# Performance work log

Measured on AMD Instinct MI355X. Metric: run time of the kernel, lower is better.

Reference implementation:

```python
import jax, jax.numpy as jnp
import numpy as np

B_SZ, C_DIM, N_DIM, S_DIM, L = 4, 512, 512, 64, 8192


def setup_inputs() -> dict:
    key = jax.random.key(0)
    ks = jax.random.split(key, 6)
    inp = jax.random.normal(ks[0], (B_SZ, C_DIM, L), dtype=jnp.float32)
    # dtA_real must be negative (exponential decay) so exp(dtA_real * l) stays bounded for l up to L
    dtA_real = -jax.random.uniform(ks[1], (N_DIM, S_DIM), dtype=jnp.float32, minval=1e-4, maxval=1e-2)
    dtA_imag = jax.random.uniform(ks[2], (N_DIM, S_DIM), dtype=jnp.float32, minval=0.0, maxval=0.1)
    Bm = jax.random.normal(ks[3], (N_DIM, C_DIM), dtype=jnp.float32) / np.float32(np.sqrt(C_DIM))
    Cm = jax.random.normal(ks[4], (C_DIM, N_DIM), dtype=jnp.float32) / np.float32(np.sqrt(N_DIM))
    E = jax.random.normal(ks[5], (N_DIM, S_DIM), dtype=jnp.float32) / np.float32(np.sqrt(S_DIM))
    return {"input": inp, "dtA_real": dtA_real, "dtA_imag": dtA_imag, "B": Bm, "C": Cm, "E": E}


def _synth_kernel(dtA_real, dtA_imag, E, length):
    # _K with complex_proj=False, weight=E, dim=-2:
    # K[n, s, l] = exp(dtA_real[n,s] * l) * cos(dtA_imag[n,s] * l); reduce over s with weight E.
    lrange = jnp.arange(length, dtype=jnp.float32)
    K = jnp.exp(dtA_real[..., None] * lrange) * jnp.cos(dtA_imag[..., None] * lrange)  # [n, s, L]
    return jnp.sum(K * E[..., None], axis=-2)  # [n, L]


def _fft_conv_dw(u, k, n):
    # real FFT causal (zero-padded to 2n) depthwise convolution: y = irfft(rfft(u) * rfft(k))[:n]
    uf = jnp.fft.rfft(u, 2 * n)          # [b, n, n+1] complex
    kf = jnp.fft.rfft(k, 2 * n)          # [n, n+1] complex, broadcast over batch
    return jnp.fft.irfft(uf * kf, 2 * n)[..., :n]


def reference(input, dtA_real, dtA_imag, B, C, E):
    n = input.shape[-1]
    # kernel synthesis (cached + detached in the torch module)
    K = jax.lax.stop_gradient(_synth_kernel(dtA_real, dtA_imag, E, n))  # [n_dim, L]
    x = jnp.einsum('bcl,nc->bnl', input, B)   # input projection
    x = _fft_conv_dw(x, K, n)                  # depthwise long conv
    return jnp.einsum('bnl,dn->bdl', x, C)     # output projection
```

## Files before the change

kernel.cpp:

```cpp
#include <hip/hip_runtime.h>
#include <hip/hip_bf16.h>

typedef unsigned short u16;
typedef __attribute__((ext_vector_type(8))) short short8;
typedef __attribute__((ext_vector_type(8))) unsigned short ushort8v;
typedef __attribute__((ext_vector_type(4))) float floatx4;

#define BSZ   4
#define CDIM  512
#define NDIM  512
#define SDIM  64
#define LEN   8192

__device__ __forceinline__ u16 f2bf(float x) {
    unsigned int u = __float_as_uint(x);
    unsigned int r = (u + 0x7FFFu + ((u >> 16) & 1u)) >> 16;
    return (u16)r;
}

#define GLL16(g, l)                                                          \
    __builtin_amdgcn_global_load_lds(                                        \
        (const __attribute__((address_space(1))) unsigned int*)(g),          \
        (__attribute__((address_space(3))) unsigned int*)(l), 16, 0, 0)

__global__ __launch_bounds__(256) void prep_nw(const float* __restrict__ dAr,
                                               const float* __restrict__ dAi,
                                               const float* __restrict__ E,
                                               u16* __restrict__ Af,
                                               u16* __restrict__ WW,
                                               const float* __restrict__ Bmf,
                                               const float* __restrict__ Cmf,
                                               u16* __restrict__ bh,
                                               u16* __restrict__ ch) {
    __shared__ float sA[64], sW[64], sE[64];
    __shared__ float Ms[128][65];
    __shared__ float sK[128];
    const int n = blockIdx.x;
    const int t = threadIdx.x;
    if (t < 64) {
        sA[t] = dAr[n * 64 + t];
        sW[t] = dAi[n * 64 + t];
        sE[t] = E[n * 64 + t];
    }
    {
        int i = n * 512 + t * 2;
        float2 vb = *(const float2*)&Bmf[i];
        float2 vc = *(const float2*)&Cmf[i];
        ushort2 hb, hc;
        hb.x = f2bf(vb.x); hb.y = f2bf(vb.y);
        hc.x = f2bf(vc.x); hc.y = f2bf(vc.y);
        *(ushort2*)&bh[i] = hb;
        *(ushort2*)&ch[i] = hc;
    }
    __syncthreads();
    u16* Afn = Af + (size_t)n * 32768;
#pragma unroll 4
    for (int it = 0; it < 32; ++it) {
        int idx = it * 256 + t;
        int tt = idx >> 6, s = idx & 63;
        float a = sA[s], w = sW[s], e = sE[s];
        float tp1 = (float)(tt + 1);
        float sn, cs;
        __sincosf(w * tp1, &sn, &cs);
        float ea = __expf(a * tp1) * e;
        float mr = ea * cs;
        Ms[tt][s] = mr;
        Afn[tt * 256 + 128 + s] = f2bf(mr);
        Afn[tt * 256 + 192 + s] = f2bf(-ea * sn);
    }
    __syncthreads();
    if (t < 128) {
        float acc = 0.f;
        if (t == 0) {
#pragma unroll
            for (int s = 0; s < 64; ++s) acc += sE[s];
        } else {
#pragma unroll
            for (int s = 0; s < 64; ++s) acc += Ms[t - 1][s];
        }
        sK[t] = acc;
    }
    __syncthreads();
#pragma unroll 8
    for (int it = 0; it < 64; ++it) {
        int idx = it * 256 + t;
        int tt = idx >> 7, k = idx & 127;
        float v = (k <= tt) ? sK[tt - k] : 0.f;
        Afn[tt * 256 + k] = f2bf(v);
    }
    u16* WWn = WW + (size_t)n * 16384;
#pragma unroll 4
    for (int it = 0; it < 32; ++it) {
        int idx = it * 256 + t;
        int s = idx >> 7, tau = idx & 127;
        float a = sA[s], w = sW[s];
        float d = (float)(127 - tau);
        float sn, cs;
        __sincosf(w * d, &sn, &cs);
        float ea = __expf(a * d);
        WWn[s * 128 + tau] = f2bf(ea * cs);
        WWn[(s + 64) * 128 + tau] = f2bf(ea * sn);
    }
}

__global__ __launch_bounds__(256) void transpose_in(const float* __restrict__ src,
                                                    u16* __restrict__ dst) {
    __shared__ float tile[64][65];
    const int b  = blockIdx.z;
    const int r0 = blockIdx.y * 64;
    const int c0 = blockIdx.x * 64;
    const int t  = threadIdx.x;
    const float* s = src + (size_t)b * 512 * 8192;
#pragma unroll
    for (int p = 0; p < 4; ++p) {
        int r = (t >> 4) + p * 16;
        float4 v = *(const float4*)&s[(size_t)(r0 + r) * 8192 + c0 + (t & 15) * 4];
        tile[r][(t & 15) * 4 + 0] = v.x;
        tile[r][(t & 15) * 4 + 1] = v.y;
        tile[r][(t & 15) * 4 + 2] = v.z;
        tile[r][(t & 15) * 4 + 3] = v.w;
    }
    __syncthreads();
#pragma unroll
    for (int p = 0; p < 4; ++p) {
        int i  = (t >> 4) + p * 16;
        int cb = (t & 15) * 4;
        ushort4 h;
        u16* hp = (u16*)&h;
#pragma unroll
        for (int q = 0; q < 4; ++q) hp[q] = f2bf(tile[cb + q][i]);
        *(ushort4*)&dst[((size_t)b * 8192 + c0 + i) * 512 + r0 + cb] = h;
    }
}

__global__ __launch_bounds__(256) void transpose_u16(const u16* __restrict__ src,
                                                     u16* __restrict__ dst) {
    __shared__ u16 tile[64][72];
    const int b  = blockIdx.z;
    const int n0 = blockIdx.y * 64;
    const int l0 = blockIdx.x * 64;
    const int t  = threadIdx.x;
    const u16* s = src + (size_t)b * 512 * 8192;
    u16* d = dst + (size_t)b * 8192 * 512;
#pragma unroll
    for (int p = 0; p < 2; ++p) {
        int r = (t >> 3) + p * 32;
        *(ushort8v*)&tile[r][(t & 7) * 8] =
            *(const ushort8v*)&s[(size_t)(n0 + r) * 8192 + l0 + (t & 7) * 8];
    }
    __syncthreads();
#pragma unroll
    for (int p = 0; p < 2; ++p) {
        int li = (t >> 3) + p * 32;
        int cb = (t & 7) * 8;
        ushort8v v;
#pragma unroll
        for (int q = 0; q < 8; ++q) v[q] = tile[cb + q][li];
        *(ushort8v*)&d[(size_t)(l0 + li) * 512 + n0 + cb] = v;
    }
}

__global__ __launch_bounds__(256) void gemm_bf16_o16(const u16* __restrict__ A,
                                                     const u16* __restrict__ Xt,
                                                     u16* __restrict__ Y) {
    __shared__ u16 As[128 * 64];
    __shared__ u16 Xs[128 * 64];
    const int b    = blockIdx.z;
    const int m0   = blockIdx.y * 128;
    const int l0   = blockIdx.x * 128;
    const int t    = threadIdx.x;
    const int w    = t >> 6;
    const int lane = t & 63;
    const int mq   = (w >> 1) * 64;
    const int lq   = (w & 1) * 64;
    const u16* Xb = Xt + (size_t)b * 8192 * 512;
    const int scol = (((lane & 7) ^ (lane >> 3)) << 3);
    const size_t a_off = (size_t)(m0 + 32 * w + (lane >> 3)) * 512 + scol;
    const size_t x_off = (size_t)(l0 + 32 * w + (lane >> 3)) * 512 + scol;
    u16* AsW = As + w * 2048;
    u16* XsW = Xs + w * 2048;

    floatx4 acc[4][4];
#pragma unroll
    for (int i = 0; i < 4; ++i)
#pragma unroll
        for (int j = 0; j < 4; ++j) acc[i][j] = (floatx4)0.f;
    const int fr = lane & 15;
    const int fk = (lane >> 4) * 8;
    const int swz = (fr & 7) << 3;

    for (int k0 = 0; k0 < 512; k0 += 64) {
        __syncthreads();
#pragma unroll
        for (int g = 0; g < 4; ++g) {
            GLL16(A + a_off + g * 4096 + k0, AsW + g * 512);
            GLL16(Xb + x_off + g * 4096 + k0, XsW + g * 512);
        }
        __syncthreads();
#pragma unroll
        for (int kk = 0; kk < 64; kk += 32) {
            short8 af[4], bf[4];
            const int pc = (kk + fk) ^ swz;
#pragma unroll
            for (int i = 0; i < 4; ++i) {
                af[i] = *(const short8*)&As[(mq + i * 16 + fr) * 64 + pc];
                bf[i] = *(const short8*)&Xs[(lq + i * 16 + fr) * 64 + pc];
            }
#pragma unroll
            for (int i = 0; i < 4; ++i)
#pragma unroll
                for (int j = 0; j < 4; ++j)
                    acc[i][j] = __builtin_amdgcn_mfma_f32_16x16x32_bf16(
                        af[i], bf[j], acc[i][j], 0, 0, 0);
        }
    }
    u16* Yb = Y + (size_t)b * 512 * 8192;
#pragma unroll
    for (int i = 0; i < 4; ++i)
#pragma unroll
        for (int j = 0; j < 4; ++j)
#pragma unroll
            for (int r = 0; r < 4; ++r) {
                int mg = m0 + mq + i * 16 + (lane >> 4) * 4 + r;
                int lg = l0 + lq + j * 16 + (lane & 15);
                Yb[(size_t)mg * 8192 + lg] = f2bf(acc[i][j][r]);
            }
}

__global__ __launch_bounds__(256) void gemm_bf16_o32(const u16* __restrict__ A,
                                                     const u16* __restrict__ Xt,
                                                     float* __restrict__ Y) {
    __shared__ u16 As[128 * 64];
    __shared__ u16 Xs[128 * 64];
    const int b    = blockIdx.z;
    const int m0   = blockIdx.y * 128;
    const int l0   = blockIdx.x * 128;
    const int t    = threadIdx.x;
    const int w    = t >> 6;
    const int lane = t & 63;
    const int mq   = (w >> 1) * 64;
    const int lq   = (w & 1) * 64;
    const u16* Xb = Xt + (size_t)b * 8192 * 512;
    const int scol = (((lane & 7) ^ (lane >> 3)) << 3);
    const size_t a_off = (size_t)(m0 + 32 * w + (lane >> 3)) * 512 + scol;
    const size_t x_off = (size_t)(l0 + 32 * w + (lane >> 3)) * 512 + scol;
    u16* AsW = As + w * 2048;
    u16* XsW = Xs + w * 2048;

    floatx4 acc[4][4];
#pragma unroll
    for (int i = 0; i < 4; ++i)
#pragma unroll
        for (int j = 0; j < 4; ++j) acc[i][j] = (floatx4)0.f;
    const int fr = lane & 15;
    const int fk = (lane >> 4) * 8;
    const int swz = (fr & 7) << 3;

    for (int k0 = 0; k0 < 512; k0 += 64) {
        __syncthreads();
#pragma unroll
        for (int g = 0; g < 4; ++g) {
            GLL16(A + a_off + g * 4096 + k0, AsW + g * 512);
            GLL16(Xb + x_off + g * 4096 + k0, XsW + g * 512);
        }
        __syncthreads();
#pragma unroll
        for (int kk = 0; kk < 64; kk += 32) {
            short8 af[4], bf[4];
            const int pc = (kk + fk) ^ swz;
#pragma unroll
            for (int i = 0; i < 4; ++i) {
                af[i] = *(const short8*)&As[(mq + i * 16 + fr) * 64 + pc];
                bf[i] = *(const short8*)&Xs[(lq + i * 16 + fr) * 64 + pc];
            }
#pragma unroll
            for (int i = 0; i < 4; ++i)
#pragma unroll
                for (int j = 0; j < 4; ++j)
                    acc[i][j] = __builtin_amdgcn_mfma_f32_16x16x32_bf16(
                        af[i], bf[j], acc[i][j], 0, 0, 0);
        }
    }
    float* Yb = Y + (size_t)b * 512 * 8192;
#pragma unroll
    for (int i = 0; i < 4; ++i)
#pragma unroll
        for (int j = 0; j < 4; ++j)
#pragma unroll
            for (int r = 0; r < 4; ++r) {
                int mg = m0 + mq + i * 16 + (lane >> 4) * 4 + r;
                int lg = l0 + lq + j * 16 + (lane & 15);
                Yb[(size_t)mg * 8192 + lg] = acc[i][j][r];
            }
}

__global__ __launch_bounds__(256) void se_gemm(const u16* __restrict__ xbf,
                                               const u16* __restrict__ WW,
                                               u16* __restrict__ SEf) {
    __shared__ u16 As[128 * 32];
    __shared__ u16 Bs[128 * 32];
    const int n  = blockIdx.y;
    const int c0 = blockIdx.x * 128;
    const int t  = threadIdx.x;
    const int w  = t >> 6, lane = t & 63;
    const int mq = (w >> 1) * 64;
    const int lq = (w & 1) * 64;
    const int ar0 = 32 * w + (lane >> 2);
    const int kq8 = (lane & 3) * 8;
    const int c_a0 = c0 + ar0, c_a1 = c_a0 + 16;
    const size_t xrow0 = ((size_t)(c_a0 >> 6) * 512 + n) * 8192 + (size_t)(c_a0 & 63) * 128 + kq8;
    const size_t xrow1 = ((size_t)(c_a1 >> 6) * 512 + n) * 8192 + (size_t)(c_a1 & 63) * 128 + kq8;
    const size_t brow0 = (size_t)n * 16384 + (size_t)ar0 * 128 + kq8;
    const size_t brow1 = brow0 + 16 * 128;
    const int wofs = w * 1024;

    floatx4 acc[4][4];
#pragma unroll
    for (int i = 0; i < 4; ++i)
#pragma unroll
        for (int j = 0; j < 4; ++j) acc[i][j] = (floatx4)0.f;
    const int fr = lane & 15, fk = (lane >> 4) * 8;

    for (int k0 = 0; k0 < 128; k0 += 32) {
        __syncthreads();
        GLL16(xbf + xrow0 + k0, As + wofs);
        GLL16(xbf + xrow1 + k0, As + wofs + 512);
        GLL16(WW + brow0 + k0, Bs + wofs);
        GLL16(WW + brow1 + k0, Bs + wofs + 512);
        __syncthreads();
        short8 af[4], bf[4];
#pragma unroll
        for (int i = 0; i < 4; ++i) {
            af[i] = *(const short8*)&As[(mq + i * 16 + fr) * 32 + fk];
            bf[i] = *(const short8*)&Bs[(lq + i * 16 + fr) * 32 + fk];
        }
#pragma unroll
        for (int i = 0; i < 4; ++i)
#pragma unroll
            for (int j = 0; j < 4; ++j)
                acc[i][j] = __builtin_amdgcn_mfma_f32_16x16x32_bf16(
                    af[i], bf[j], acc[i][j], 0, 0, 0);
    }
#pragma unroll
    for (int i = 0; i < 4; ++i)
#pragma unroll
        for (int j = 0; j < 4; ++j)
#pragma unroll
            for (int r = 0; r < 4; ++r) {
                int c = c0 + mq + i * 16 + (lane >> 4) * 4 + r;
                int q = lq + j * 16 + (lane & 15);
                SEf[(((size_t)(c >> 6) * 512 + n) * 64 + (c & 63)) * 128 + q] =
                    f2bf(acc[i][j][r]);
            }
}

__global__ __launch_bounds__(256) void bscan(const float* __restrict__ dAr,
                                             const float* __restrict__ dAi,
                                             const u16* __restrict__ SEf,
                                             u16* __restrict__ Ht) {
    const int id = blockIdx.x * 256 + threadIdx.x;
    const int s = id & 63, n = (id >> 6) & 511, b = id >> 15;
    const float a = dAr[n * 64 + s], wv = dAi[n * 64 + s];
    const float eaT = expf(a * 128.f);
    float sT, cT;
    sincosf(wv * 128.f, &sT, &cT);
    const float zTr = eaT * cT, zTi = eaT * sT;
    const size_t base = ((size_t)b * 512 + n) * 64 * 128;
    float Hr = 0.f, Hi = 0.f;
    for (int j = 0; j < 64; ++j) {
        Ht[base + j * 128 + s]      = f2bf(Hr);
        Ht[base + j * 128 + 64 + s] = f2bf(Hi);
        float ser = __uint_as_float((unsigned int)SEf[base + j * 128 + s] << 16);
        float sei = __uint_as_float((unsigned int)SEf[base + j * 128 + 64 + s] << 16);
        float nHr = fmaf(zTr, Hr, fmaf(-zTi, Hi, ser));
        float nHi = fmaf(zTi, Hr, fmaf(zTr, Hi, sei));
        Hr = nHr; Hi = nHi;
    }
}

__global__ __launch_bounds__(256) void y_gemm(const u16* __restrict__ xbf,
                                              const u16* __restrict__ Ht,
                                              const u16* __restrict__ Af,
                                              u16* __restrict__ wyb) {
    __shared__ u16 As[128 * 32];
    __shared__ u16 Bs[128 * 32];
    const int n  = blockIdx.y;
    const int c0 = blockIdx.x * 128;
    const int t  = threadIdx.x;
    const int w  = t >> 6, lane = t & 63;
    const int mq = (w >> 1) * 64;
    const int lq = (w & 1) * 64;
    const int ar0 = 32 * w + (lane >> 2);
    const int kq8 = (lane & 3) * 8;
    const int c_a0 = c0 + ar0, c_a1 = c_a0 + 16;
    const size_t xrow0 = ((size_t)(c_a0 >> 6) * 512 + n) * 8192 + (size_t)(c_a0 & 63) * 128 + kq8;
    const size_t xrow1 = ((size_t)(c_a1 >> 6) * 512 + n) * 8192 + (size_t)(c_a1 & 63) * 128 + kq8;
    const size_t hrow0 = (((size_t)(c_a0 >> 6) * 512 + n) * 64 + (c_a0 & 63)) * 128 + kq8;
    const size_t hrow1 = (((size_t)(c_a1 >> 6) * 512 + n) * 64 + (c_a1 & 63)) * 128 + kq8;
    const size_t brow0 = (size_t)n * 32768 + (size_t)ar0 * 256 + kq8;
    const size_t brow1 = brow0 + 16 * 256;
    const int wofs = w * 1024;

    floatx4 acc[4][4];
#pragma unroll
    for (int i = 0; i < 4; ++i)
#pragma unroll
        for (int j = 0; j < 4; ++j) acc[i][j] = (floatx4)0.f;
    const int fr = lane & 15, fk = (lane >> 4) * 8;

    for (int k0 = 0; k0 < 256; k0 += 32) {
        __syncthreads();
        if (k0 < 128) {
            GLL16(xbf + xrow0 + k0, As + wofs);
            GLL16(xbf + xrow1 + k0, As + wofs + 512);
        } else {
            GLL16(Ht + hrow0 + (k0 - 128), As + wofs);
            GLL16(Ht + hrow1 + (k0 - 128), As + wofs + 512);
        }
        GLL16(Af + brow0 + k0, Bs + wofs);
        GLL16(Af + brow1 + k0, Bs + wofs + 512);
        __syncthreads();
        short8 af[4], bf[4];
#pragma unroll
        for (int i = 0; i < 4; ++i) {
            af[i] = *(const short8*)&As[(mq + i * 16 + fr) * 32 + fk];
            bf[i] = *(const short8*)&Bs[(lq + i * 16 + fr) * 32 + fk];
        }
#pragma unroll
        for (int i = 0; i < 4; ++i)
#pragma unroll
            for (int j = 0; j < 4; ++j)
                acc[i][j] = __builtin_amdgcn_mfma_f32_16x16x32_bf16(
                    af[i], bf[j], acc[i][j], 0, 0, 0);
    }
#pragma unroll
    for (int i = 0; i < 4; ++i)
#pragma unroll
        for (int j = 0; j < 4; ++j)
#pragma unroll
            for (int r = 0; r < 4; ++r) {
                int c  = c0 + mq + i * 16 + (lane >> 4) * 4 + r;
                int tc = lq + j * 16 + (lane & 15);
                wyb[((size_t)(c >> 6) * 512 + n) * 8192 + (size_t)(c & 63) * 128 + tc] =
                    f2bf(acc[i][j][r]);
            }
}

extern "C" void kernel_launch(void* const* d_in, const int* in_sizes, int n_in,
                              void* d_out, int out_size, void* d_ws, size_t ws_size,
                              hipStream_t stream) {
    const float* input = (const float*)d_in[0];
    const float* dAr   = (const float*)d_in[1];
    const float* dAi   = (const float*)d_in[2];
    const float* Bm    = (const float*)d_in[3];
    const float* Cm    = (const float*)d_in[4];
    const float* E     = (const float*)d_in[5];
    float* out = (float*)d_out;

    char* ws = (char*)d_ws;
    const size_t MB = 1048576;
    u16* xt   = (u16*)(ws + 0);
    u16* xbf  = (u16*)(ws + 32 * MB);
    u16* Af   = (u16*)(ws + 64 * MB);
    u16* WW   = (u16*)(ws + 96 * MB);
    u16* SEf  = (u16*)(ws + 112 * MB);
    u16* Ht   = (u16*)(ws + 144 * MB);
    u16* Bmb  = (u16*)(ws + 176 * MB);
    u16* Cmb  = (u16*)(ws + 177 * MB);
    u16* wyb  = xt;
    u16* yt   = xbf;

    prep_nw<<<512, 256, 0, stream>>>(dAr, dAi, E, Af, WW, Bm, Cm, Bmb, Cmb);
    transpose_in<<<dim3(128, 8, BSZ), 256, 0, stream>>>(input, xt);
    gemm_bf16_o16<<<dim3(64, 4, BSZ), 256, 0, stream>>>(Bmb, xt, xbf);
    se_gemm<<<dim3(2, 512), 256, 0, stream>>>(xbf, WW, SEf);
    bscan<<<512, 256, 0, stream>>>(dAr, dAi, SEf, Ht);
    y_gemm<<<dim3(2, 512), 256, 0, stream>>>(xbf, Ht, Af, wyb);
    transpose_u16<<<dim3(128, 8, BSZ), 256, 0, stream>>>(wyb, yt);
    gemm_bf16_o32<<<dim3(64, 4, BSZ), 256, 0, stream>>>(Cmb, yt, out);
}
```

Measured before the change: 268.1 us.

## Merge prep with input transpose and double M tile in se/y GEMMs

Folds the parameter-prep kernel and the input transpose into one launch, dispatching on block index, so one kernel launch and its tail are removed. Doubles the per-block M tile in se_gemm and y_gemm from 128 to 256 rows (8x4 accumulators per wave), so each B tile loaded into LDS is reused twice as much and the grid shrinks from 1024 to 512 blocks. The trade is higher register pressure, lower occupancy and fewer blocks in flight.

```diff
diff --git a/kernel.cpp b/kernel.cpp
--- a/kernel.cpp
+++ b/kernel.cpp
@@ -23,113 +23,118 @@
         (const __attribute__((address_space(1))) unsigned int*)(g),          \
         (__attribute__((address_space(3))) unsigned int*)(l), 16, 0, 0)
 
-__global__ __launch_bounds__(256) void prep_nw(const float* __restrict__ dAr,
-                                               const float* __restrict__ dAi,
-                                               const float* __restrict__ E,
-                                               u16* __restrict__ Af,
-                                               u16* __restrict__ WW,
-                                               const float* __restrict__ Bmf,
-                                               const float* __restrict__ Cmf,
-                                               u16* __restrict__ bh,
-                                               u16* __restrict__ ch) {
-    __shared__ float sA[64], sW[64], sE[64];
-    __shared__ float Ms[128][65];
-    __shared__ float sK[128];
-    const int n = blockIdx.x;
+__global__ __launch_bounds__(256) void prep_all(const float* __restrict__ dAr,
+                                                const float* __restrict__ dAi,
+                                                const float* __restrict__ E,
+                                                u16* __restrict__ Af,
+                                                u16* __restrict__ WW,
+                                                const float* __restrict__ Bmf,
+                                                const float* __restrict__ Cmf,
+                                                u16* __restrict__ bh,
+                                                u16* __restrict__ ch,
+                                                const float* __restrict__ input,
+                                                u16* __restrict__ xt) {
+    __shared__ __align__(16) char smem[34816];
+    const int bid = blockIdx.x;
     const int t = threadIdx.x;
-    if (t < 64) {
-        sA[t] = dAr[n * 64 + t];
-        sW[t] = dAi[n * 64 + t];
-        sE[t] = E[n * 64 + t];
-    }
-    {
-        int i = n * 512 + t * 2;
-        float2 vb = *(const float2*)&Bmf[i];
-        float2 vc = *(const float2*)&Cmf[i];
-        ushort2 hb, hc;
-        hb.x = f2bf(vb.x); hb.y = f2bf(vb.y);
-        hc.x = f2bf(vc.x); hc.y = f2bf(vc.y);
-        *(ushort2*)&bh[i] = hb;
-        *(ushort2*)&ch[i] = hc;
-    }
-    __syncthreads();
-    u16* Afn = Af + (size_t)n * 32768;
+    if (bid < 512) {
+        float* sA = (float*)smem;
+        float* sW = sA + 64;
+        float* sE = sW + 64;
+        float* sK = sE + 64;
+        float (*Ms)[65] = (float (*)[65])(sK + 128);
+        const int n = bid;
+        if (t < 64) {
+            sA[t] = dAr[n * 64 + t];
+            sW[t] = dAi[n * 64 + t];
+            sE[t] = E[n * 64 + t];
+        }
+        {
+            int i = n * 512 + t * 2;
+            float2 vb = *(const float2*)&Bmf[i];
+            float2 vc = *(const float2*)&Cmf[i];
+            ushort2 hb, hc;
+            hb.x = f2bf(vb.x); hb.y = f2bf(vb.y);
+            hc.x = f2bf(vc.x); hc.y = f2bf(vc.y);
+            *(ushort2*)&bh[i] = hb;
+            *(ushort2*)&ch[i] = hc;
+        }
+        __syncthreads();
+        u16* Afn = Af + (size_t)n * 32768;
 #pragma unroll 4
-    for (int it = 0; it < 32; ++it) {
-        int idx = it * 256 + t;
-        int tt = idx >> 6, s = idx & 63;
-        float a = sA[s], w = sW[s], e = sE[s];
-        float tp1 = (float)(tt + 1);
-        float sn, cs;
-        __sincosf(w * tp1, &sn, &cs);
-        float ea = __expf(a * tp1) * e;
-        float mr = ea * cs;
-        Ms[tt][s] = mr;
-        Afn[tt * 256 + 128 + s] = f2bf(mr);
-        Afn[tt * 256 + 192 + s] = f2bf(-ea * sn);
-    }
-    __syncthreads();
-    if (t < 128) {
-        float acc = 0.f;
-        if (t == 0) {
-#pragma unroll
-            for (int s = 0; s < 64; ++s) acc += sE[s];
-        } else {
-#pragma unroll
-            for (int s = 0; s < 64; ++s) acc += Ms[t - 1][s];
-        }
-        sK[t] = acc;
-    }
-    __syncthreads();
+        for (int it = 0; it < 32; ++it) {
+            int idx = it * 256 + t;
+            int tt = idx >> 6, s = idx & 63;
+            float a = sA[s], w = sW[s], e = sE[s];
+            float tp1 = (float)(tt + 1);
+            float sn, cs;
+            __sincosf(w * tp1, &sn, &cs);
+            float ea = __expf(a * tp1) * e;
+            float mr = ea * cs;
+            Ms[tt][s] = mr;
+            Afn[tt * 256 + 128 + s] = f2bf(mr);
+            Afn[tt * 256 + 192 + s] = f2bf(-ea * sn);
+        }
+        __syncthreads();
+        if (t < 128) {
+            float acc = 0.f;
+            if (t == 0) {
+#pragma unroll
+                for (int s = 0; s < 64; ++s) acc += sE[s];
+            } else {
+#pragma unroll
+                for (int s = 0; s < 64; ++s) acc += Ms[t - 1][s];
+            }
+            sK[t] = acc;
+        }
+        __syncthreads();
 #pragma unroll 8
-    for (int it = 0; it < 64; ++it) {
-        int idx = it * 256 + t;
-        int tt = idx >> 7, k = idx & 127;
-        float v = (k <= tt) ? sK[tt - k] : 0.f;
-        Afn[tt * 256 + k] = f2bf(v);
-    }
-    u16* WWn = WW + (size_t)n * 16384;
+        for (int it = 0; it < 64; ++it) {
+            int idx = it * 256 + t;
+            int tt = idx >> 7, k = idx & 127;
+            float v = (k <= tt) ? sK[tt - k] : 0.f;
+            Afn[tt * 256 + k] = f2bf(v);
+        }
+        u16* WWn = WW + (size_t)n * 16384;
 #pragma unroll 4
-    for (int it = 0; it < 32; ++it) {
-        int idx = it * 256 + t;
-        int s = idx >> 7, tau = idx & 127;
-        float a = sA[s], w = sW[s];
-        float d = (float)(127 - tau);
-        float sn, cs;
-        __sincosf(w * d, &sn, &cs);
-        float ea = __expf(a * d);
-        WWn[s * 128 + tau] = f2bf(ea * cs);
-        WWn[(s + 64) * 128 + tau] = f2bf(ea * sn);
-    }
-}
-
-__global__ __launch_bounds__(256) void transpose_in(const float* __restrict__ src,
-                                                    u16* __restrict__ dst) {
-    __shared__ float tile[64][65];
-    const int b  = blockIdx.z;
-    const int r0 = blockIdx.y * 64;
-    const int c0 = blockIdx.x * 64;
-    const int t  = threadIdx.x;
-    const float* s = src + (size_t)b * 512 * 8192;
-#pragma unroll
-    for (int p = 0; p < 4; ++p) {
-        int r = (t >> 4) + p * 16;
-        float4 v = *(const float4*)&s[(size_t)(r0 + r) * 8192 + c0 + (t & 15) * 4];
-        tile[r][(t & 15) * 4 + 0] = v.x;
-        tile[r][(t & 15) * 4 + 1] = v.y;
-        tile[r][(t & 15) * 4 + 2] = v.z;
-        tile[r][(t & 15) * 4 + 3] = v.w;
-    }
-    __syncthreads();
-#pragma unroll
-    for (int p = 0; p < 4; ++p) {
-        int i  = (t >> 4) + p * 16;
-        int cb = (t & 15) * 4;
-        ushort4 h;
-        u16* hp = (u16*)&h;
-#pragma unroll
-        for (int q = 0; q < 4; ++q) hp[q] = f2bf(tile[cb + q][i]);
-        *(ushort4*)&dst[((size_t)b * 8192 + c0 + i) * 512 + r0 + cb] = h;
+        for (int it = 0; it < 32; ++it) {
+            int idx = it * 256 + t;
+            int s = idx >> 7, tau = idx & 127;
+            float a = sA[s], w = sW[s];
+            float d = (float)(127 - tau);
+            float sn, cs;
+            __sincosf(w * d, &sn, &cs);
+            float ea = __expf(a * d);
+            WWn[s * 128 + tau] = f2bf(ea * cs);
+            WWn[(s + 64) * 128 + tau] = f2bf(ea * sn);
+        }
+    } else {
+        float (*tile)[65] = (float (*)[65])smem;
+        const int tid = bid - 512;
+        const int b  = tid >> 10;
+        const int r0 = ((tid >> 7) & 7) * 64;
+        const int c0 = (tid & 127) * 64;
+        const float* s = input + (size_t)b * 512 * 8192;
+#pragma unroll
+        for (int p = 0; p < 4; ++p) {
+            int r = (t >> 4) + p * 16;
+            float4 v = *(const float4*)&s[(size_t)(r0 + r) * 8192 + c0 + (t & 15) * 4];
+            tile[r][(t & 15) * 4 + 0] = v.x;
+            tile[r][(t & 15) * 4 + 1] = v.y;
+            tile[r][(t & 15) * 4 + 2] = v.z;
+            tile[r][(t & 15) * 4 + 3] = v.w;
+        }
+        __syncthreads();
+#pragma unroll
+        for (int p = 0; p < 4; ++p) {
+            int i  = (t >> 4) + p * 16;
+            int cb = (t & 15) * 4;
+            ushort4 h;
+            u16* hp = (u16*)&h;
+#pragma unroll
+            for (int q = 0; q < 4; ++q) hp[q] = f2bf(tile[cb + q][i]);
+            *(ushort4*)&xt[((size_t)b * 8192 + c0 + i) * 512 + r0 + cb] = h;
+        }
     }
 }
 
@@ -297,58 +302,62 @@
 __global__ __launch_bounds__(256) void se_gemm(const u16* __restrict__ xbf,
                                                const u16* __restrict__ WW,
                                                u16* __restrict__ SEf) {
-    __shared__ u16 As[128 * 32];
+    __shared__ u16 As[256 * 32];
     __shared__ u16 Bs[128 * 32];
-    const int n  = blockIdx.y;
-    const int c0 = blockIdx.x * 128;
+    const int n  = blockIdx.x;
     const int t  = threadIdx.x;
     const int w  = t >> 6, lane = t & 63;
-    const int mq = (w >> 1) * 64;
+    const int mq = (w >> 1) * 128;
     const int lq = (w & 1) * 64;
-    const int ar0 = 32 * w + (lane >> 2);
+    const int ar0 = 64 * w + (lane >> 2);
     const int kq8 = (lane & 3) * 8;
-    const int c_a0 = c0 + ar0, c_a1 = c_a0 + 16;
-    const size_t xrow0 = ((size_t)(c_a0 >> 6) * 512 + n) * 8192 + (size_t)(c_a0 & 63) * 128 + kq8;
-    const size_t xrow1 = ((size_t)(c_a1 >> 6) * 512 + n) * 8192 + (size_t)(c_a1 & 63) * 128 + kq8;
-    const size_t brow0 = (size_t)n * 16384 + (size_t)ar0 * 128 + kq8;
+    size_t xrow[4];
+#pragma unroll
+    for (int g = 0; g < 4; ++g) {
+        int c = ar0 + 16 * g;
+        xrow[g] = ((size_t)(c >> 6) * 512 + n) * 8192 + (size_t)(c & 63) * 128 + kq8;
+    }
+    const size_t brow0 = (size_t)n * 16384 + (size_t)(32 * w + (lane >> 2)) * 128 + kq8;
     const size_t brow1 = brow0 + 16 * 128;
-    const int wofs = w * 1024;
-
-    floatx4 acc[4][4];
-#pragma unroll
-    for (int i = 0; i < 4; ++i)
+    const int wofsA = w * 2048;
+    const int wofsB = w * 1024;
+    const int fr = lane & 15, fk = (lane >> 4) * 8;
+
+    floatx4 acc[8][4];
+#pragma unroll
+    for (int i = 0; i < 8; ++i)
 #pragma unroll
         for (int j = 0; j < 4; ++j) acc[i][j] = (floatx4)0.f;
-    const int fr = lane & 15, fk = (lane >> 4) * 8;
 
     for (int k0 = 0; k0 < 128; k0 += 32) {
         __syncthreads();
-        GLL16(xbf + xrow0 + k0, As + wofs);
-        GLL16(xbf + xrow1 + k0, As + wofs + 512);
-        GLL16(WW + brow0 + k0, Bs + wofs);
-        GLL16(WW + brow1 + k0, Bs + wofs + 512);
-        __syncthreads();
-        short8 af[4], bf[4];
-#pragma unroll
-        for (int i = 0; i < 4; ++i) {
-            af[i] = *(const short8*)&As[(mq + i * 16 + fr) * 32 + fk];
-            bf[i] = *(const short8*)&Bs[(lq + i * 16 + fr) * 32 + fk];
-        }
-#pragma unroll
-        for (int i = 0; i < 4; ++i)
+#pragma unroll
+        for (int g = 0; g < 4; ++g)
+            GLL16(xbf + xrow[g] + k0, As + wofsA + g * 512);
+        GLL16(WW + brow0 + k0, Bs + wofsB);
+        GLL16(WW + brow1 + k0, Bs + wofsB + 512);
+        __syncthreads();
+        short8 bfr[4];
+#pragma unroll
+        for (int j = 0; j < 4; ++j)
+            bfr[j] = *(const short8*)&Bs[(lq + j * 16 + fr) * 32 + fk];
+#pragma unroll
+        for (int i = 0; i < 8; ++i) {
+            short8 af = *(const short8*)&As[(mq + i * 16 + fr) * 32 + fk];
 #pragma unroll
             for (int j = 0; j < 4; ++j)
                 acc[i][j] = __builtin_amdgcn_mfma_f32_16x16x32_bf16(
-                    af[i], bf[j], acc[i][j], 0, 0, 0);
-    }
-#pragma unroll
-    for (int i = 0; i < 4; ++i)
+                    af, bfr[j], acc[i][j], 0, 0, 0);
+        }
+    }
+#pragma unroll
+    for (int i = 0; i < 8; ++i)
 #pragma unroll
         for (int j = 0; j < 4; ++j)
 #pragma unroll
             for (int r = 0; r < 4; ++r) {
-                int c = c0 + mq + i * 16 + (lane >> 4) * 4 + r;
-                int q = lq + j * 16 + (lane & 15);
+                int c = mq + i * 16 + (lane >> 4) * 4 + r;
+                int q = lq + j * 16 + fr;
                 SEf[(((size_t)(c >> 6) * 512 + n) * 64 + (c & 63)) * 128 + q] =
                     f2bf(acc[i][j][r]);
             }
@@ -382,65 +391,69 @@
                                               const u16* __restrict__ Ht,
                                               const u16* __restrict__ Af,
                                               u16* __restrict__ wyb) {
-    __shared__ u16 As[128 * 32];
+    __shared__ u16 As[256 * 32];
     __shared__ u16 Bs[128 * 32];
-    const int n  = blockIdx.y;
-    const int c0 = blockIdx.x * 128;
+    const int n  = blockIdx.x;
     const int t  = threadIdx.x;
     const int w  = t >> 6, lane = t & 63;
-    const int mq = (w >> 1) * 64;
+    const int mq = (w >> 1) * 128;
     const int lq = (w & 1) * 64;
-    const int ar0 = 32 * w + (lane >> 2);
+    const int ar0 = 64 * w + (lane >> 2);
     const int kq8 = (lane & 3) * 8;
-    const int c_a0 = c0 + ar0, c_a1 = c_a0 + 16;
-    const size_t xrow0 = ((size_t)(c_a0 >> 6) * 512 + n) * 8192 + (size_t)(c_a0 & 63) * 128 + kq8;
-    const size_t xrow1 = ((size_t)(c_a1 >> 6) * 512 + n) * 8192 + (size_t)(c_a1 & 63) * 128 + kq8;
-    const size_t hrow0 = (((size_t)(c_a0 >> 6) * 512 + n) * 64 + (c_a0 & 63)) * 128 + kq8;
-    const size_t hrow1 = (((size_t)(c_a1 >> 6) * 512 + n) * 64 + (c_a1 & 63)) * 128 + kq8;
-    const size_t brow0 = (size_t)n * 32768 + (size_t)ar0 * 256 + kq8;
+    size_t xrow[4], hrow[4];
+#pragma unroll
+    for (int g = 0; g < 4; ++g) {
+        int c = ar0 + 16 * g;
+        xrow[g] = ((size_t)(c >> 6) * 512 + n) * 8192 + (size_t)(c & 63) * 128 + kq8;
+        hrow[g] = (((size_t)(c >> 6) * 512 + n) * 64 + (c & 63)) * 128 + kq8;
+    }
+    const size_t brow0 = (size_t)n * 32768 + (size_t)(32 * w + (lane >> 2)) * 256 + kq8;
     const size_t brow1 = brow0 + 16 * 256;
-    const int wofs = w * 1024;
-
-    floatx4 acc[4][4];
-#pragma unroll
-    for (int i = 0; i < 4; ++i)
+    const int wofsA = w * 2048;
+    const int wofsB = w * 1024;
+    const int fr = lane & 15, fk = (lane >> 4) * 8;
+
+    floatx4 acc[8][4];
+#pragma unroll
+    for (int i = 0; i < 8; ++i)
 #pragma unroll
         for (int j = 0; j < 4; ++j) acc[i][j] = (floatx4)0.f;
-    const int fr = lane & 15, fk = (lane >> 4) * 8;
 
     for (int k0 = 0; k0 < 256; k0 += 32) {
         __syncthreads();
         if (k0 < 128) {
-            GLL16(xbf + xrow0 + k0, As + wofs);
-            GLL16(xbf + xrow1 + k0, As + wofs + 512);
+#pragma unroll
+            for (int g = 0; g < 4; ++g)
+                GLL16(xbf + xrow[g] + k0, As + wofsA + g * 512);
         } else {
-            GLL16(Ht + hrow0 + (k0 - 128), As + wofs);
-            GLL16(Ht + hrow1 + (k0 - 128), As + wofs + 512);
-        }
-        GLL16(Af + brow0 + k0, Bs + wofs);
-        GLL16(Af + brow1 + k0, Bs + wofs + 512);
-        __syncthreads();
-        short8 af[4], bf[4];
-#pragma unroll
-        for (int i = 0; i < 4; ++i) {
-            af[i] = *(const short8*)&As[(mq + i * 16 + fr) * 32 + fk];
-            bf[i] = *(const short8*)&Bs[(lq + i * 16 + fr) * 32 + fk];
-        }
-#pragma unroll
-        for (int i = 0; i < 4; ++i)
+#pragma unroll
+            for (int g = 0; g < 4; ++g)
+                GLL16(Ht + hrow[g] + (k0 - 128), As + wofsA + g * 512);
+        }
+        GLL16(Af + brow0 + k0, Bs + wofsB);
+        GLL16(Af + brow1 + k0, Bs + wofsB + 512);
+        __syncthreads();
+        short8 bfr[4];
+#pragma unroll
+        for (int j = 0; j < 4; ++j)
+            bfr[j] = *(const short8*)&Bs[(lq + j * 16 + fr) * 32 + fk];
+#pragma unroll
+        for (int i = 0; i < 8; ++i) {
+            short8 af = *(const short8*)&As[(mq + i * 16 + fr) * 32 + fk];
 #pragma unroll
             for (int j = 0; j < 4; ++j)
                 acc[i][j] = __builtin_amdgcn_mfma_f32_16x16x32_bf16(
-                    af[i], bf[j], acc[i][j], 0, 0, 0);
-    }
-#pragma unroll
-    for (int i = 0; i < 4; ++i)
+                    af, bfr[j], acc[i][j], 0, 0, 0);
+        }
+    }
+#pragma unroll
+    for (int i = 0; i < 8; ++i)
 #pragma unroll
         for (int j = 0; j < 4; ++j)
 #pragma unroll
             for (int r = 0; r < 4; ++r) {
-                int c  = c0 + mq + i * 16 + (lane >> 4) * 4 + r;
-                int tc = lq + j * 16 + (lane & 15);
+                int c  = mq + i * 16 + (lane >> 4) * 4 + r;
+                int tc = lq + j * 16 + fr;
                 wyb[((size_t)(c >> 6) * 512 + n) * 8192 + (size_t)(c & 63) * 128 + tc] =
                     f2bf(acc[i][j][r]);
             }
@@ -470,12 +483,12 @@
     u16* wyb  = xt;
     u16* yt   = xbf;
 
-    prep_nw<<<512, 256, 0, stream>>>(dAr, dAi, E, Af, WW, Bm, Cm, Bmb, Cmb);
-    transpose_in<<<dim3(128, 8, BSZ), 256, 0, stream>>>(input, xt);
+    prep_all<<<4608, 256, 0, stream>>>(dAr, dAi, E, Af, WW, Bm, Cm, Bmb, Cmb,
+                                       input, xt);
     gemm_bf16_o16<<<dim3(64, 4, BSZ), 256, 0, stream>>>(Bmb, xt, xbf);
-    se_gemm<<<dim3(2, 512), 256, 0, stream>>>(xbf, WW, SEf);
+    se_gemm<<<512, 256, 0, stream>>>(xbf, WW, SEf);
     bscan<<<512, 256, 0, stream>>>(dAr, dAi, SEf, Ht);
-    y_gemm<<<dim3(2, 512), 256, 0, stream>>>(xbf, Ht, Af, wyb);
+    y_gemm<<<512, 256, 0, stream>>>(xbf, Ht, Af, wyb);
     transpose_u16<<<dim3(128, 8, BSZ), 256, 0, stream>>>(wyb, yt);
     gemm_bf16_o32<<<dim3(64, 4, BSZ), 256, 0, stream>>>(Cmb, yt, out);
 }
```

Result: faster. 243.8 us (-9.1%).
